# Kernel optimization log

Hardware: AMD Instinct MI355X
Metric: run time of the kernel (lower is better)

Reference implementation:

```python
import jax, jax.numpy as jnp
import numpy as np

N_NODES = 100000
N_EDGES = 1700000


def _build_csr(rng, n, e):
    row = rng.integers(0, n, size=e).astype(np.int64)
    col = rng.integers(0, n, size=e).astype(np.int32)
    order = np.argsort(row, kind='stable')
    row = row[order]
    col = col[order]
    rowptr = np.searchsorted(row, np.arange(n + 1)).astype(np.int32)
    return rowptr, col


def setup_inputs() -> dict:
    key = jax.random.key(0)
    k1, k2, k3, k4 = jax.random.split(key, 4)
    rng = np.random.default_rng(0)
    rowptr, colind = _build_csr(rng, N_NODES, N_EDGES)
    F_in, H, C = 256, 128, 16
    return {
        'x': jax.random.normal(k1, (N_NODES, F_in), dtype=jnp.float32),
        'edge_weight': jax.random.uniform(k2, (N_EDGES,), dtype=jnp.float32) + 0.5,
        'W1': jax.random.normal(k3, (F_in, H), dtype=jnp.float32) * (1.0 / np.sqrt(F_in)),
        'b1': jnp.zeros((H,), dtype=jnp.float32),
        'W2': jax.random.normal(k4, (H, C), dtype=jnp.float32) * (1.0 / np.sqrt(H)),
        'b2': jnp.zeros((C,), dtype=jnp.float32),
        'rowptr': jnp.asarray(rowptr),
        'colind': jnp.asarray(colind),
    }


def _rowids_from_rowptr(rowptr, n_edges):
    # CSR rowptr -> per-nnz row index, jit-friendly
    return (jnp.searchsorted(rowptr, jnp.arange(n_edges, dtype=rowptr.dtype), side='right') - 1).astype(jnp.int32)


def reference(x, edge_weight, W1, b1, W2, b2, rowptr, colind):
    n = x.shape[0]
    e = colind.shape[0]
    row = _rowids_from_rowptr(rowptr, e)
    col = colind

    # GCN symmetric normalization: D^-1/2 A D^-1/2 (cached=True -> shared by both layers)
    deg = jax.ops.segment_sum(edge_weight, row, num_segments=n)
    dinv = jnp.where(deg > 0, jax.lax.rsqrt(deg), 0.0)
    w = dinv[row] * edge_weight * dinv[col]

    def gcn_layer(h, W, b):
        h = h @ W                                   # [n, d_out]
        # SpMM: out[r] = sum_e w[e] * h[col[e]]
        msg = w[:, None] * h[col]                   # [e, d_out] gather
        return jax.ops.segment_sum(msg, row, num_segments=n) + b

    h = jax.nn.relu(gcn_layer(x, W1, b1))
    # dropout is identity in eval mode
    out = gcn_layer(h, W2, b2)
    return jax.nn.log_softmax(out, axis=1)
```

## Files before the change

### kernel.cpp

```cpp
#include <hip/hip_runtime.h>
#include <hip/hip_bf16.h>

#define F_IN 256
#define HDIM 128
#define CDIM 16

typedef unsigned short u16;
typedef unsigned int u32;

typedef __attribute__((ext_vector_type(8))) short bf16x8;
typedef __attribute__((ext_vector_type(4))) float f32x4;

__device__ __forceinline__ float bf2f(u32 v) {
    u32 u = v << 16;
    float f;
    __builtin_memcpy(&f, &u, 4);
    return f;
}
__device__ __forceinline__ float asf(u32 u) {
    float f;
    __builtin_memcpy(&f, &u, 4);
    return f;
}
__device__ __forceinline__ u16 f2bf(float f) {
    u32 u;
    __builtin_memcpy(&u, &f, 4);
    u32 r = (u + 0x7FFFu + ((u >> 16) & 1u)) >> 16;
    return (u16)r;
}
__device__ __forceinline__ u32 cvtpk(float lo, float hi) {
    u32 r;
    asm("v_cvt_pk_bf16_f32 %0, %1, %2" : "=v"(r) : "v"(lo), "v"(hi));
    return r;
}

__global__ __launch_bounds__(256) void k_dinv(const float* __restrict__ ew,
                                              const int* __restrict__ rowptr,
                                              float* __restrict__ dinv, int n) {
    int sg = threadIdx.x >> 4;
    int sl = threadIdx.x & 15;
    int r = blockIdx.x * 16 + sg;
    if (r >= n) return;
    int s = rowptr[r], e = rowptr[r + 1];
    float acc = 0.f;
    for (int i = s + sl; i < e; i += 16) acc += ew[i];
    acc += __shfl_xor(acc, 1);
    acc += __shfl_xor(acc, 2);
    acc += __shfl_xor(acc, 4);
    acc += __shfl_xor(acc, 8);
    if (sl == 0) dinv[r] = (acc > 0.f) ? rsqrtf(acc) : 0.f;
}

__global__ __launch_bounds__(256) void k_w(const float* __restrict__ ew,
                                           const int* __restrict__ rowptr,
                                           const int* __restrict__ col,
                                           const float* __restrict__ dinv,
                                           float* __restrict__ wn, int n) {
    int sg = threadIdx.x >> 4;
    int sl = threadIdx.x & 15;
    int r = blockIdx.x * 16 + sg;
    if (r >= n) return;
    float dr = dinv[r];
    int s = rowptr[r], e = rowptr[r + 1];
    for (int i = s + sl; i < e; i += 16)
        wn[i] = dr * ew[i] * dinv[col[i]];
}

__global__ void k_prepw1(const float* __restrict__ W1, u16* __restrict__ W1T) {
    int idx = blockIdx.x * blockDim.x + threadIdx.x;
    if (idx >= HDIM * F_IN) return;
    int f = idx >> 8;
    int k = idx & 255;
    W1T[idx] = f2bf(W1[(size_t)k * HDIM + f]);
}

__global__ __launch_bounds__(512, 4) void k_gemm1(const float* __restrict__ x,
                                                  const u16* __restrict__ W1T,
                                                  u16* __restrict__ T1, int n) {
    __shared__ u16 Bs[HDIM * F_IN];

    int tid = threadIdx.x;
#pragma unroll
    for (int it = 0; it < 8; it++) {
        int o16 = it * 512 + tid;
        u32 o = (u32)o16 * 16;
        u32 swz = o ^ (((o >> 9) & 7u) << 4);
        uint4 v = ((const uint4*)W1T)[o16];
        *(uint4*)((char*)Bs + swz) = v;
    }
    __syncthreads();

    int wave = tid >> 6;
    int lane = tid & 63;
    int lr = lane & 15;
    int kg = lane >> 4;
    int r0 = blockIdx.x * 256 + wave * 32;
    if (r0 >= n) return;

    f32x4 acc[2][8];
#pragma unroll
    for (int rg = 0; rg < 2; rg++)
#pragma unroll
        for (int ct = 0; ct < 8; ct++) acc[rg][ct] = (f32x4){0.f, 0.f, 0.f, 0.f};

    const float* arow[2];
#pragma unroll
    for (int rg = 0; rg < 2; rg++) {
        int row = r0 + rg * 16 + lr;
        arow[rg] = x + (size_t)(row < n ? row : (n - 1)) * F_IN + kg * 8;
    }

    float4 laA[2], haA[2], laB[2], haB[2];

#define LOADA(L_, H_, kkv_) do { \
        _Pragma("unroll") \
        for (int rg = 0; rg < 2; rg++) { \
            const float4* ap = (const float4*)(arow[rg] + (kkv_) * 32); \
            L_[rg] = ap[0]; H_[rg] = ap[1]; \
        } } while (0)

#define COMPUTE(L_, H_, kkv_) do { \
        bf16x8 afrag[2]; \
        _Pragma("unroll") \
        for (int rg = 0; rg < 2; rg++) { \
            u32 qa[4]; \
            qa[0] = cvtpk(L_[rg].x, L_[rg].y); \
            qa[1] = cvtpk(L_[rg].z, L_[rg].w); \
            qa[2] = cvtpk(H_[rg].x, H_[rg].y); \
            qa[3] = cvtpk(H_[rg].z, H_[rg].w); \
            __builtin_memcpy(&afrag[rg], qa, 16); \
        } \
        _Pragma("unroll") \
        for (int ct = 0; ct < 8; ct++) { \
            u32 a = (u32)(ct * 16 + lr) * (F_IN * 2) + (u32)kg * 16 + (u32)(kkv_) * 64; \
            u32 aswz = a ^ (((a >> 9) & 7u) << 4); \
            bf16x8 bfrag = *(const bf16x8*)((const char*)Bs + aswz); \
            _Pragma("unroll") \
            for (int rg = 0; rg < 2; rg++) \
                acc[rg][ct] = __builtin_amdgcn_mfma_f32_16x16x32_bf16(afrag[rg], bfrag, acc[rg][ct], 0, 0, 0); \
        } } while (0)

    LOADA(laA, haA, 0);
#pragma unroll
    for (int kk = 0; kk < 8; kk += 2) {
        LOADA(laB, haB, kk + 1);
        COMPUTE(laA, haA, kk);
        if (kk + 2 < 8) LOADA(laA, haA, kk + 2);
        COMPUTE(laB, haB, kk + 1);
    }
#undef LOADA
#undef COMPUTE

#pragma unroll
    for (int rg = 0; rg < 2; rg++) {
        int rbase = r0 + rg * 16 + kg * 4;
#pragma unroll
        for (int ct = 0; ct < 8; ct++) {
#pragma unroll
            for (int i = 0; i < 4; i += 2) {
                u32 q = cvtpk(acc[rg][ct][i], acc[rg][ct][i + 1]);
                int row0 = rbase + i;
                int row1 = rbase + i + 1;
                if (row0 < n) T1[(size_t)row0 * HDIM + ct * 16 + lr] = (u16)(q & 0xFFFFu);
                if (row1 < n) T1[(size_t)row1 * HDIM + ct * 16 + lr] = (u16)(q >> 16);
            }
        }
    }
}

__global__ __launch_bounds__(256) void k_spmm1(const u16* __restrict__ T1,
                                               const float* __restrict__ wn,
                                               const int* __restrict__ rowptr,
                                               const int* __restrict__ col,
                                               const float* __restrict__ b1,
                                               u16* __restrict__ H, int n) {
    int wave = threadIdx.x >> 6;
    int lane = threadIdx.x & 63;
    int r = blockIdx.x * 4 + wave;
    if (r >= n) return;
    int es = lane >> 4;
    int fl = lane & 15;

    int s = rowptr[r], e = rowptr[r + 1];
    int deg = e - s;
    int nwin = deg >> 4;
    float a[8];
#pragma unroll
    for (int j = 0; j < 8; j++) a[j] = 0.f;

#define ACCUM(w_, p_) do { \
        a[0] += (w_) * asf((p_).x << 16); a[1] += (w_) * asf((p_).x & 0xFFFF0000u); \
        a[2] += (w_) * asf((p_).y << 16); a[3] += (w_) * asf((p_).y & 0xFFFF0000u); \
        a[4] += (w_) * asf((p_).z << 16); a[5] += (w_) * asf((p_).z & 0xFFFF0000u); \
        a[6] += (w_) * asf((p_).w << 16); a[7] += (w_) * asf((p_).w & 0xFFFF0000u); \
    } while (0)

    int i = s + es;
    for (int w = 0; w < nwin; w++, i += 16) {
        float w0 = wn[i];      int c0 = col[i];
        float w1 = wn[i + 4];  int c1 = col[i + 4];
        float w2 = wn[i + 8];  int c2 = col[i + 8];
        float w3 = wn[i + 12]; int c3 = col[i + 12];
        uint4 p0 = *(const uint4*)(T1 + (size_t)c0 * HDIM + fl * 8);
        uint4 p1 = *(const uint4*)(T1 + (size_t)c1 * HDIM + fl * 8);
        uint4 p2 = *(const uint4*)(T1 + (size_t)c2 * HDIM + fl * 8);
        uint4 p3 = *(const uint4*)(T1 + (size_t)c3 * HDIM + fl * 8);
        ACCUM(w0, p0);
        ACCUM(w1, p1);
        ACCUM(w2, p2);
        ACCUM(w3, p3);
    }
    if (deg & 15) {
        int i1 = i + 4, i2 = i + 8, i3 = i + 12;
        int j0 = i  < e ? i  : (e - 1);
        int j1 = i1 < e ? i1 : (e - 1);
        int j2 = i2 < e ? i2 : (e - 1);
        int j3 = i3 < e ? i3 : (e - 1);
        float w0 = i  < e ? wn[j0] : 0.f;
        float w1 = i1 < e ? wn[j1] : 0.f;
        float w2 = i2 < e ? wn[j2] : 0.f;
        float w3 = i3 < e ? wn[j3] : 0.f;
        int c0 = col[j0], c1 = col[j1], c2 = col[j2], c3 = col[j3];
        uint4 p0 = *(const uint4*)(T1 + (size_t)c0 * HDIM + fl * 8);
        uint4 p1 = *(const uint4*)(T1 + (size_t)c1 * HDIM + fl * 8);
        uint4 p2 = *(const uint4*)(T1 + (size_t)c2 * HDIM + fl * 8);
        uint4 p3 = *(const uint4*)(T1 + (size_t)c3 * HDIM + fl * 8);
        ACCUM(w0, p0);
        ACCUM(w1, p1);
        ACCUM(w2, p2);
        ACCUM(w3, p3);
    }
#undef ACCUM

#pragma unroll
    for (int j = 0; j < 8; j++) {
        a[j] += __shfl_xor(a[j], 16);
        a[j] += __shfl_xor(a[j], 32);
    }

    if (es == 0) {
        const float4* bb = (const float4*)(b1 + fl * 8);
        float4 blo = bb[0], bhi = bb[1];
        float v0 = a[0] + blo.x, v1 = a[1] + blo.y;
        float v2 = a[2] + blo.z, v3 = a[3] + blo.w;
        float v4 = a[4] + bhi.x, v5 = a[5] + bhi.y;
        float v6 = a[6] + bhi.z, v7 = a[7] + bhi.w;
        v0 = v0 > 0.f ? v0 : 0.f; v1 = v1 > 0.f ? v1 : 0.f;
        v2 = v2 > 0.f ? v2 : 0.f; v3 = v3 > 0.f ? v3 : 0.f;
        v4 = v4 > 0.f ? v4 : 0.f; v5 = v5 > 0.f ? v5 : 0.f;
        v6 = v6 > 0.f ? v6 : 0.f; v7 = v7 > 0.f ? v7 : 0.f;
        uint4 o;
        o.x = cvtpk(v0, v1); o.y = cvtpk(v2, v3);
        o.z = cvtpk(v4, v5); o.w = cvtpk(v6, v7);
        *(uint4*)(H + (size_t)r * HDIM + fl * 8) = o;
    }
}

__global__ __launch_bounds__(256) void k_gemm2(const u16* __restrict__ H,
                                               const float* __restrict__ W2,
                                               float* __restrict__ U, int n) {
    int rl = threadIdx.x >> 4;
    int f = threadIdx.x & 15;
    int row = blockIdx.x * 16 + rl;
    if (row >= n) return;
    const u32* hr = (const u32*)(H + (size_t)row * HDIM);
    float acc = 0.f;
    for (int k2 = 0; k2 < HDIM / 2; k2++) {
        u32 pr = hr[k2];
        float h0 = asf(pr << 16);
        float h1 = asf(pr & 0xFFFF0000u);
        acc += h0 * W2[(size_t)(k2 * 2) * CDIM + f];
        acc += h1 * W2[(size_t)(k2 * 2 + 1) * CDIM + f];
    }
    U[(size_t)row * CDIM + f] = acc;
}

__global__ __launch_bounds__(256) void k_out(const float* __restrict__ U,
                                             const float* __restrict__ wn,
                                             const int* __restrict__ rowptr,
                                             const int* __restrict__ col,
                                             const float* __restrict__ b2,
                                             float* __restrict__ out, int n) {
    int wave = threadIdx.x >> 6;
    int lane = threadIdx.x & 63;
    int r = blockIdx.x * 4 + wave;
    if (r >= n) return;
    int es = lane >> 3;
    int fl = lane & 7;
    int s = rowptr[r], e = rowptr[r + 1];
    int deg = e - s;
    int nwin = deg >> 4;
    float a0 = 0.f, a1 = 0.f;

    int i = s + es;
    for (int w = 0; w < nwin; w++, i += 16) {
        float w0 = wn[i];     int c0 = col[i];
        float w1 = wn[i + 8]; int c1 = col[i + 8];
        float2 u0 = *(const float2*)(U + (size_t)c0 * CDIM + fl * 2);
        float2 u1 = *(const float2*)(U + (size_t)c1 * CDIM + fl * 2);
        a0 += w0 * u0.x; a1 += w0 * u0.y;
        a0 += w1 * u1.x; a1 += w1 * u1.y;
    }
    if (deg & 15) {
        int i1 = i + 8;
        int j0 = i  < e ? i  : (e - 1);
        int j1 = i1 < e ? i1 : (e - 1);
        float w0 = i  < e ? wn[j0] : 0.f;
        float w1 = i1 < e ? wn[j1] : 0.f;
        int c0 = col[j0], c1 = col[j1];
        float2 u0 = *(const float2*)(U + (size_t)c0 * CDIM + fl * 2);
        float2 u1 = *(const float2*)(U + (size_t)c1 * CDIM + fl * 2);
        a0 += w0 * u0.x; a1 += w0 * u0.y;
        a0 += w1 * u1.x; a1 += w1 * u1.y;
    }

    a0 += __shfl_xor(a0, 8);  a1 += __shfl_xor(a1, 8);
    a0 += __shfl_xor(a0, 16); a1 += __shfl_xor(a1, 16);
    a0 += __shfl_xor(a0, 32); a1 += __shfl_xor(a1, 32);

    float2 bp = ((const float2*)b2)[fl];
    float v0 = a0 + bp.x;
    float v1 = a1 + bp.y;

    float m = fmaxf(v0, v1);
    m = fmaxf(m, __shfl_xor(m, 1));
    m = fmaxf(m, __shfl_xor(m, 2));
    m = fmaxf(m, __shfl_xor(m, 4));
    float ss = __expf(v0 - m) + __expf(v1 - m);
    ss += __shfl_xor(ss, 1);
    ss += __shfl_xor(ss, 2);
    ss += __shfl_xor(ss, 4);
    float ls = __logf(ss);
    if (es == 0) {
        float2 res = {v0 - m - ls, v1 - m - ls};
        *(float2*)(out + (size_t)r * CDIM + fl * 2) = res;
    }
}

extern "C" void kernel_launch(void* const* d_in, const int* in_sizes, int n_in,
                              void* d_out, int out_size, void* d_ws, size_t ws_size,
                              hipStream_t stream) {
    const float* x      = (const float*)d_in[0];
    const float* ew     = (const float*)d_in[1];
    const float* W1     = (const float*)d_in[2];
    const float* b1     = (const float*)d_in[3];
    const float* W2     = (const float*)d_in[4];
    const float* b2     = (const float*)d_in[5];
    const int*   rowptr = (const int*)d_in[6];
    const int*   colind = (const int*)d_in[7];

    int n = in_sizes[6] - 1;
    int E = in_sizes[7];

    auto align256 = [](size_t v) { return (v + 255) & ~(size_t)255; };
    char* p = (char*)d_ws;
    float* dinv = (float*)p; p += align256((size_t)n * 4);
    float* wn   = (float*)p; p += align256((size_t)E * 4);
    u16*   T1   = (u16*)p;   p += align256((size_t)n * HDIM * 2);
    u16*   H    = (u16*)p;   p += align256((size_t)n * HDIM * 2);
    float* U    = (float*)p; p += align256((size_t)n * CDIM * 4);
    u16*   W1T  = (u16*)p;   p += align256((size_t)HDIM * F_IN * 2);
    float* out  = (float*)d_out;

    k_dinv<<<(n + 15) / 16, 256, 0, stream>>>(ew, rowptr, dinv, n);
    k_w<<<(n + 15) / 16, 256, 0, stream>>>(ew, rowptr, colind, dinv, wn, n);
    k_prepw1<<<(HDIM * F_IN + 255) / 256, 256, 0, stream>>>(W1, W1T);

    k_gemm1<<<(n + 255) / 256, 512, 0, stream>>>(x, W1T, T1, n);

    k_spmm1<<<(n + 3) / 4, 256, 0, stream>>>(T1, wn, rowptr, colind, b1, H, n);
    k_gemm2<<<(n + 15) / 16, 256, 0, stream>>>(H, W2, U, n);
    k_out<<<(n + 3) / 4, 256, 0, stream>>>(U, wn, rowptr, colind, b2, out, n);
}
```

Measured before the change: 180.3 us.

## Fuse second-layer GEMM into first SpMM epilogue, drop hidden buffer

The H·W2 projection now runs inside the first SpMM kernel's epilogue. Each wave takes its reduced 128-wide hidden row, applies bias and ReLU, multiplies by W2 using lane-distributed partial dot products, reduces with shuffles and writes the 16-wide U row directly. This removes the bf16 H write and reread and one kernel launch. H also stays in fp32 instead of being rounded to bf16. The cost is extra shuffles and W2 loads inside the latency-bound gather kernel.

```diff
diff --git a/kernel.cpp b/kernel.cpp
--- a/kernel.cpp
+++ b/kernel.cpp
@@ -173,7 +173,8 @@
                                                const int* __restrict__ rowptr,
                                                const int* __restrict__ col,
                                                const float* __restrict__ b1,
-                                               u16* __restrict__ H, int n) {
+                                               const float* __restrict__ W2,
+                                               float* __restrict__ U, int n) {
     int wave = threadIdx.x >> 6;
     int lane = threadIdx.x & 63;
     int r = blockIdx.x * 4 + wave;
@@ -238,41 +239,35 @@
         a[j] += __shfl_xor(a[j], 32);
     }
 
-    if (es == 0) {
-        const float4* bb = (const float4*)(b1 + fl * 8);
-        float4 blo = bb[0], bhi = bb[1];
-        float v0 = a[0] + blo.x, v1 = a[1] + blo.y;
-        float v2 = a[2] + blo.z, v3 = a[3] + blo.w;
-        float v4 = a[4] + bhi.x, v5 = a[5] + bhi.y;
-        float v6 = a[6] + bhi.z, v7 = a[7] + bhi.w;
-        v0 = v0 > 0.f ? v0 : 0.f; v1 = v1 > 0.f ? v1 : 0.f;
-        v2 = v2 > 0.f ? v2 : 0.f; v3 = v3 > 0.f ? v3 : 0.f;
-        v4 = v4 > 0.f ? v4 : 0.f; v5 = v5 > 0.f ? v5 : 0.f;
-        v6 = v6 > 0.f ? v6 : 0.f; v7 = v7 > 0.f ? v7 : 0.f;
-        uint4 o;
-        o.x = cvtpk(v0, v1); o.y = cvtpk(v2, v3);
-        o.z = cvtpk(v4, v5); o.w = cvtpk(v6, v7);
-        *(uint4*)(H + (size_t)r * HDIM + fl * 8) = o;
-    }
-}
-
-__global__ __launch_bounds__(256) void k_gemm2(const u16* __restrict__ H,
-                                               const float* __restrict__ W2,
-                                               float* __restrict__ U, int n) {
-    int rl = threadIdx.x >> 4;
-    int f = threadIdx.x & 15;
-    int row = blockIdx.x * 16 + rl;
-    if (row >= n) return;
-    const u32* hr = (const u32*)(H + (size_t)row * HDIM);
-    float acc = 0.f;
-    for (int k2 = 0; k2 < HDIM / 2; k2++) {
-        u32 pr = hr[k2];
-        float h0 = asf(pr << 16);
-        float h1 = asf(pr & 0xFFFF0000u);
-        acc += h0 * W2[(size_t)(k2 * 2) * CDIM + f];
-        acc += h1 * W2[(size_t)(k2 * 2 + 1) * CDIM + f];
-    }
-    U[(size_t)row * CDIM + f] = acc;
+    const float4* bb = (const float4*)(b1 + fl * 8);
+    float4 blo = bb[0], bhi = bb[1];
+    float v[8];
+    v[0] = a[0] + blo.x; v[1] = a[1] + blo.y;
+    v[2] = a[2] + blo.z; v[3] = a[3] + blo.w;
+    v[4] = a[4] + bhi.x; v[5] = a[5] + bhi.y;
+    v[6] = a[6] + bhi.z; v[7] = a[7] + bhi.w;
+#pragma unroll
+    for (int j = 0; j < 8; j++) v[j] = v[j] > 0.f ? v[j] : 0.f;
+
+    float4 p = {0.f, 0.f, 0.f, 0.f};
+#pragma unroll
+    for (int j = 0; j < 8; j++) {
+        float4 w = *(const float4*)(W2 + (size_t)(fl * 8 + j) * CDIM + es * 4);
+        p.x += v[j] * w.x;
+        p.y += v[j] * w.y;
+        p.z += v[j] * w.z;
+        p.w += v[j] * w.w;
+    }
+#pragma unroll
+    for (int d = 1; d < 16; d <<= 1) {
+        p.x += __shfl_xor(p.x, d);
+        p.y += __shfl_xor(p.y, d);
+        p.z += __shfl_xor(p.z, d);
+        p.w += __shfl_xor(p.w, d);
+    }
+    if (fl == 0) {
+        *(float4*)(U + (size_t)r * CDIM + es * 4) = p;
+    }
 }
 
 __global__ __launch_bounds__(256) void k_out(const float* __restrict__ U,
@@ -357,7 +352,6 @@
     float* dinv = (float*)p; p += align256((size_t)n * 4);
     float* wn   = (float*)p; p += align256((size_t)E * 4);
     u16*   T1   = (u16*)p;   p += align256((size_t)n * HDIM * 2);
-    u16*   H    = (u16*)p;   p += align256((size_t)n * HDIM * 2);
     float* U    = (float*)p; p += align256((size_t)n * CDIM * 4);
     u16*   W1T  = (u16*)p;   p += align256((size_t)HDIM * F_IN * 2);
     float* out  = (float*)d_out;
@@ -368,7 +362,6 @@
 
     k_gemm1<<<(n + 255) / 256, 512, 0, stream>>>(x, W1T, T1, n);
 
-    k_spmm1<<<(n + 3) / 4, 256, 0, stream>>>(T1, wn, rowptr, colind, b1, H, n);
-    k_gemm2<<<(n + 15) / 16, 256, 0, stream>>>(H, W2, U, n);
+    k_spmm1<<<(n + 3) / 4, 256, 0, stream>>>(T1, wn, rowptr, colind, b1, W2, U, n);
     k_out<<<(n + 3) / 4, 256, 0, stream>>>(U, wn, rowptr, colind, b2, out, n);
 }
```

Measured after the change: 206.2 us. 14.3% more time.

## Fold edge normalization into SpMM kernels and merge prep launches

Applied to the files above, without the earlier changes.

Drops the separate kernel that materialized per-edge normalized weights and instead computes dr*ew*dinv[col] inline inside both SpMM kernels. The degree and W1 transpose/convert kernels are merged into one launch with a block-index split. This removes one E-sized write pass and two launches. In exchange it adds an extra random gather of dinv[col] per edge in each SpMM.

```diff
diff --git a/kernel.cpp b/kernel.cpp
--- a/kernel.cpp
+++ b/kernel.cpp
@@ -34,9 +34,21 @@
     return r;
 }
 
-__global__ __launch_bounds__(256) void k_dinv(const float* __restrict__ ew,
-                                              const int* __restrict__ rowptr,
-                                              float* __restrict__ dinv, int n) {
+__global__ __launch_bounds__(256) void k_pre(const float* __restrict__ ew,
+                                             const int* __restrict__ rowptr,
+                                             const float* __restrict__ W1,
+                                             float* __restrict__ dinv,
+                                             u16* __restrict__ W1T,
+                                             int n, int nbd) {
+    if ((int)blockIdx.x >= nbd) {
+        int idx = ((int)blockIdx.x - nbd) * 256 + threadIdx.x;
+        if (idx < HDIM * F_IN) {
+            int f = idx >> 8;
+            int k = idx & 255;
+            W1T[idx] = f2bf(W1[(size_t)k * HDIM + f]);
+        }
+        return;
+    }
     int sg = threadIdx.x >> 4;
     int sl = threadIdx.x & 15;
     int r = blockIdx.x * 16 + sg;
@@ -49,29 +61,6 @@
     acc += __shfl_xor(acc, 4);
     acc += __shfl_xor(acc, 8);
     if (sl == 0) dinv[r] = (acc > 0.f) ? rsqrtf(acc) : 0.f;
-}
-
-__global__ __launch_bounds__(256) void k_w(const float* __restrict__ ew,
-                                           const int* __restrict__ rowptr,
-                                           const int* __restrict__ col,
-                                           const float* __restrict__ dinv,
-                                           float* __restrict__ wn, int n) {
-    int sg = threadIdx.x >> 4;
-    int sl = threadIdx.x & 15;
-    int r = blockIdx.x * 16 + sg;
-    if (r >= n) return;
-    float dr = dinv[r];
-    int s = rowptr[r], e = rowptr[r + 1];
-    for (int i = s + sl; i < e; i += 16)
-        wn[i] = dr * ew[i] * dinv[col[i]];
-}
-
-__global__ void k_prepw1(const float* __restrict__ W1, u16* __restrict__ W1T) {
-    int idx = blockIdx.x * blockDim.x + threadIdx.x;
-    if (idx >= HDIM * F_IN) return;
-    int f = idx >> 8;
-    int k = idx & 255;
-    W1T[idx] = f2bf(W1[(size_t)k * HDIM + f]);
 }
 
 __global__ __launch_bounds__(512, 4) void k_gemm1(const float* __restrict__ x,
@@ -169,7 +158,8 @@
 }
 
 __global__ __launch_bounds__(256) void k_spmm1(const u16* __restrict__ T1,
-                                               const float* __restrict__ wn,
+                                               const float* __restrict__ ew,
+                                               const float* __restrict__ dinv,
                                                const int* __restrict__ rowptr,
                                                const int* __restrict__ col,
                                                const float* __restrict__ b1,
@@ -184,6 +174,7 @@
     int s = rowptr[r], e = rowptr[r + 1];
     int deg = e - s;
     int nwin = deg >> 4;
+    float dr = dinv[r];
     float a[8];
 #pragma unroll
     for (int j = 0; j < 8; j++) a[j] = 0.f;
@@ -197,14 +188,18 @@
 
     int i = s + es;
     for (int w = 0; w < nwin; w++, i += 16) {
-        float w0 = wn[i];      int c0 = col[i];
-        float w1 = wn[i + 4];  int c1 = col[i + 4];
-        float w2 = wn[i + 8];  int c2 = col[i + 8];
-        float w3 = wn[i + 12]; int c3 = col[i + 12];
+        float e0 = ew[i];      int c0 = col[i];
+        float e1 = ew[i + 4];  int c1 = col[i + 4];
+        float e2 = ew[i + 8];  int c2 = col[i + 8];
+        float e3 = ew[i + 12]; int c3 = col[i + 12];
         uint4 p0 = *(const uint4*)(T1 + (size_t)c0 * HDIM + fl * 8);
         uint4 p1 = *(const uint4*)(T1 + (size_t)c1 * HDIM + fl * 8);
         uint4 p2 = *(const uint4*)(T1 + (size_t)c2 * HDIM + fl * 8);
         uint4 p3 = *(const uint4*)(T1 + (size_t)c3 * HDIM + fl * 8);
+        float w0 = dr * e0 * dinv[c0];
+        float w1 = dr * e1 * dinv[c1];
+        float w2 = dr * e2 * dinv[c2];
+        float w3 = dr * e3 * dinv[c3];
         ACCUM(w0, p0);
         ACCUM(w1, p1);
         ACCUM(w2, p2);
@@ -216,11 +211,11 @@
         int j1 = i1 < e ? i1 : (e - 1);
         int j2 = i2 < e ? i2 : (e - 1);
         int j3 = i3 < e ? i3 : (e - 1);
-        float w0 = i  < e ? wn[j0] : 0.f;
-        float w1 = i1 < e ? wn[j1] : 0.f;
-        float w2 = i2 < e ? wn[j2] : 0.f;
-        float w3 = i3 < e ? wn[j3] : 0.f;
         int c0 = col[j0], c1 = col[j1], c2 = col[j2], c3 = col[j3];
+        float w0 = i  < e ? dr * ew[j0] * dinv[c0] : 0.f;
+        float w1 = i1 < e ? dr * ew[j1] * dinv[c1] : 0.f;
+        float w2 = i2 < e ? dr * ew[j2] * dinv[c2] : 0.f;
+        float w3 = i3 < e ? dr * ew[j3] * dinv[c3] : 0.f;
         uint4 p0 = *(const uint4*)(T1 + (size_t)c0 * HDIM + fl * 8);
         uint4 p1 = *(const uint4*)(T1 + (size_t)c1 * HDIM + fl * 8);
         uint4 p2 = *(const uint4*)(T1 + (size_t)c2 * HDIM + fl * 8);
@@ -276,7 +271,8 @@
 }
 
 __global__ __launch_bounds__(256) void k_out(const float* __restrict__ U,
-                                             const float* __restrict__ wn,
+                                             const float* __restrict__ ew,
+                                             const float* __restrict__ dinv,
                                              const int* __restrict__ rowptr,
                                              const int* __restrict__ col,
                                              const float* __restrict__ b2,
@@ -290,14 +286,17 @@
     int s = rowptr[r], e = rowptr[r + 1];
     int deg = e - s;
     int nwin = deg >> 4;
+    float dr = dinv[r];
     float a0 = 0.f, a1 = 0.f;
 
     int i = s + es;
     for (int w = 0; w < nwin; w++, i += 16) {
-        float w0 = wn[i];     int c0 = col[i];
-        float w1 = wn[i + 8]; int c1 = col[i + 8];
+        float e0 = ew[i];     int c0 = col[i];
+        float e1 = ew[i + 8]; int c1 = col[i + 8];
         float2 u0 = *(const float2*)(U + (size_t)c0 * CDIM + fl * 2);
         float2 u1 = *(const float2*)(U + (size_t)c1 * CDIM + fl * 2);
+        float w0 = dr * e0 * dinv[c0];
+        float w1 = dr * e1 * dinv[c1];
         a0 += w0 * u0.x; a1 += w0 * u0.y;
         a0 += w1 * u1.x; a1 += w1 * u1.y;
     }
@@ -305,9 +304,9 @@
         int i1 = i + 8;
         int j0 = i  < e ? i  : (e - 1);
         int j1 = i1 < e ? i1 : (e - 1);
-        float w0 = i  < e ? wn[j0] : 0.f;
-        float w1 = i1 < e ? wn[j1] : 0.f;
         int c0 = col[j0], c1 = col[j1];
+        float w0 = i  < e ? dr * ew[j0] * dinv[c0] : 0.f;
+        float w1 = i1 < e ? dr * ew[j1] * dinv[c1] : 0.f;
         float2 u0 = *(const float2*)(U + (size_t)c0 * CDIM + fl * 2);
         float2 u1 = *(const float2*)(U + (size_t)c1 * CDIM + fl * 2);
         a0 += w0 * u0.x; a1 += w0 * u0.y;
@@ -351,24 +350,23 @@
 
     int n = in_sizes[6] - 1;
     int E = in_sizes[7];
+    (void)E;
 
     auto align256 = [](size_t v) { return (v + 255) & ~(size_t)255; };
     char* p = (char*)d_ws;
     float* dinv = (float*)p; p += align256((size_t)n * 4);
-    float* wn   = (float*)p; p += align256((size_t)E * 4);
     u16*   T1   = (u16*)p;   p += align256((size_t)n * HDIM * 2);
     u16*   H    = (u16*)p;   p += align256((size_t)n * HDIM * 2);
     float* U    = (float*)p; p += align256((size_t)n * CDIM * 4);
     u16*   W1T  = (u16*)p;   p += align256((size_t)HDIM * F_IN * 2);
     float* out  = (float*)d_out;
 
-    k_dinv<<<(n + 15) / 16, 256, 0, stream>>>(ew, rowptr, dinv, n);
-    k_w<<<(n + 15) / 16, 256, 0, stream>>>(ew, rowptr, colind, dinv, wn, n);
-    k_prepw1<<<(HDIM * F_IN + 255) / 256, 256, 0, stream>>>(W1, W1T);
+    int nbd = (n + 15) / 16;
+    k_pre<<<nbd + 128, 256, 0, stream>>>(ew, rowptr, W1, dinv, W1T, n, nbd);
 
     k_gemm1<<<(n + 255) / 256, 512, 0, stream>>>(x, W1T, T1, n);
 
-    k_spmm1<<<(n + 3) / 4, 256, 0, stream>>>(T1, wn, rowptr, colind, b1, H, n);
+    k_spmm1<<<(n + 3) / 4, 256, 0, stream>>>(T1, ew, dinv, rowptr, colind, b1, H, n);
     k_gemm2<<<(n + 15) / 16, 256, 0, stream>>>(H, W2, U, n);
-    k_out<<<(n + 3) / 4, 256, 0, stream>>>(U, wn, rowptr, colind, b2, out, n);
-}
+    k_out<<<(n + 3) / 4, 256, 0, stream>>>(U, ew, dinv, rowptr, colind, b2, out, n);
+}
```

After: 177.6 us. About the same (-1.5%).
